# Performance work log

Measured on AMD Instinct MI355X. Metric: run time of the kernel, lower is better.

The kernel has to match this reference:

```python
import jax, jax.numpy as jnp
import numpy as np

B = 65536      # batch
S = 256        # state_dim
A = 8          # n_agents
NA = 16        # n_actions
K = 10         # num_kernel
H = 64         # adv_hypernet_embed
AD = A * NA    # action_dim
D = S + AD     # state_dim + action_dim


def setup_inputs() -> dict:
    key = jax.random.key(0)
    ks = jax.random.split(key, 20)
    sc = 0.05
    inp = {
        'states': jax.random.normal(ks[0], (B, S), jnp.float32),
        'actions_onehot': jax.random.uniform(ks[1], (B, A, NA), jnp.float32),
        # key extractors: S -> H -> H -> 1, stacked over K kernels
        'kW1': jax.random.normal(ks[2], (K, H, S), jnp.float32) * sc,
        'kb1': jnp.zeros((K, H), jnp.float32),
        'kW2': jax.random.normal(ks[3], (K, H, H), jnp.float32) * sc,
        'kb2': jnp.zeros((K, H), jnp.float32),
        'kW3': jax.random.normal(ks[4], (K, 1, H), jnp.float32) * sc,
        'kb3': jnp.zeros((K, 1), jnp.float32),
        # agents extractors: S -> H -> H -> A
        'aW1': jax.random.normal(ks[5], (K, H, S), jnp.float32) * sc,
        'ab1': jnp.zeros((K, H), jnp.float32),
        'aW2': jax.random.normal(ks[6], (K, H, H), jnp.float32) * sc,
        'ab2': jnp.zeros((K, H), jnp.float32),
        'aW3': jax.random.normal(ks[7], (K, A, H), jnp.float32) * sc,
        'ab3': jnp.zeros((K, A), jnp.float32),
        # action extractors: S+AD -> H -> H -> A
        'cW1': jax.random.normal(ks[8], (K, H, D), jnp.float32) * sc,
        'cb1': jnp.zeros((K, H), jnp.float32),
        'cW2': jax.random.normal(ks[9], (K, H, H), jnp.float32) * sc,
        'cb2': jnp.zeros((K, H), jnp.float32),
        'cW3': jax.random.normal(ks[10], (K, A, H), jnp.float32) * sc,
        'cb3': jnp.zeros((K, A), jnp.float32),
    }
    return inp


def _mlp3(x, W1, b1, W2, b2, W3, b3):
    # x: [B, in] ; W1: [K, H, in] -> batched over K kernels in one GEMM
    h = jax.nn.relu(jnp.einsum('bd,khd->bkh', x, W1) + b1)        # [B,K,H]
    h = jax.nn.relu(jnp.einsum('bkh,kgh->bkg', h, W2) + b2)       # [B,K,H]
    return jnp.einsum('bkh,koh->bko', h, W3) + b3                 # [B,K,out]


def reference(states, actions_onehot,
              kW1, kb1, kW2, kb2, kW3, kb3,
              aW1, ab1, aW2, ab2, aW3, ab3,
              cW1, cb1, cW2, cb2, cW3, cb3):
    actions_flat = actions_onehot.reshape(states.shape[0], -1)    # [B, A*NA]
    data = jnp.concatenate([states, actions_flat], axis=1)        # [B, S+AD]

    x_key = jnp.abs(_mlp3(states, kW1, kb1, kW2, kb2, kW3, kb3)) + 1e-10   # [B,K,1]
    x_agents = jax.nn.sigmoid(_mlp3(states, aW1, ab1, aW2, ab2, aW3, ab3)) # [B,K,A]
    x_action = jax.nn.sigmoid(_mlp3(data, cW1, cb1, cW2, cb2, cW3, cb3))   # [B,K,A]

    # broadcast key over agents, multiply gates, sum over the K kernels
    head_attend = jnp.sum(x_key * x_agents * x_action, axis=1)    # [B,A]
    return head_attend
```

## Files before the change

### kernel.cpp

```cpp
#include <hip/hip_runtime.h>
#include <hip/hip_bf16.h>

#define Bsz 65536
#define Sdim 256
#define Aag 8
#define NAct 16
#define Kk 10
#define Hh 64
#define ADdim 128
#define Ddim 384

#define OFF_KW1 0
#define OFF_AW1 16384
#define OFF_CW1 32768
#define OFF_KW2 57344
#define OFF_AW2 61440
#define OFF_CW2 65536
#define OFF_KW3 69632
#define OFF_AW3 70656
#define OFF_CW3 71680
#define SLAB 72704

typedef float f32x4 __attribute__((ext_vector_type(4)));
typedef __bf16 bf16x8 __attribute__((ext_vector_type(8)));

#define MFMA(a, b, cacc) __builtin_amdgcn_mfma_f32_16x16x32_bf16((a), (b), (cacc), 0, 0, 0)

__device__ __forceinline__ __bf16 f2bf(float f) {
    unsigned int u = __float_as_uint(f);
    unsigned int r = (u + 0x7fffu + ((u >> 16) & 1u)) >> 16;
    union { unsigned short s; __bf16 b; } cv;
    cv.s = (unsigned short)r;
    return cv.b;
}

__global__ void prep_weights(const float* __restrict__ kW1, const float* __restrict__ aW1,
                             const float* __restrict__ cW1, const float* __restrict__ kW2,
                             const float* __restrict__ aW2, const float* __restrict__ cW2,
                             const float* __restrict__ kW3, const float* __restrict__ aW3,
                             const float* __restrict__ cW3, __bf16* __restrict__ out) {
    int gid = blockIdx.x * 256 + threadIdx.x;
    if (gid >= SLAB * Kk) return;
    int k = gid / SLAB;
    int off = gid - k * SLAB;
    float v;
    if (off < OFF_AW1)        v = kW1[k * 16384 + off];
    else if (off < OFF_CW1)   v = aW1[k * 16384 + off - OFF_AW1];
    else if (off < OFF_KW2)   v = cW1[k * 24576 + off - OFF_CW1];
    else if (off < OFF_AW2)   v = kW2[k * 4096 + off - OFF_KW2];
    else if (off < OFF_CW2)   v = aW2[k * 4096 + off - OFF_AW2];
    else if (off < OFF_KW3)   v = cW2[k * 4096 + off - OFF_CW2];
    else if (off < OFF_AW3) { int r = off - OFF_KW3; v = (r < 64)  ? kW3[k * 64 + r]  : 0.0f; }
    else if (off < OFF_CW3) { int r = off - OFF_AW3; v = (r < 512) ? aW3[k * 512 + r] : 0.0f; }
    else                    { int r = off - OFF_CW3; v = (r < 512) ? cW3[k * 512 + r] : 0.0f; }
    out[gid] = f2bf(v);
}

template <int KN>
__device__ __forceinline__ void stage_net(const __bf16* __restrict__ w1src,
                                          const __bf16* __restrict__ w2src,
                                          const __bf16* __restrict__ w3src,
                                          __bf16* W1s, __bf16* W2s, __bf16* W3s, int tid) {
    __syncthreads();
    constexpr int STR = KN + 8;
    constexpr int CPR = KN / 8;
    constexpr int N1 = 64 * CPR;
#pragma unroll 4
    for (int ci = tid; ci < N1; ci += 256) {
        int row = ci / CPR;
        int cc = ci - row * CPR;
        *(float4*)(W1s + row * STR + cc * 8) = *(const float4*)(w1src + row * KN + cc * 8);
    }
    {
        int ci = tid;
#pragma unroll
        for (int it = 0; it < 2; ++it, ci += 256) {
            int row = ci >> 3, cc = ci & 7;
            *(float4*)(W2s + row * 72 + cc * 8) = *(const float4*)(w2src + row * 64 + cc * 8);
        }
    }
    if (tid < 128) {
        int row = tid >> 3, cc = tid & 7;
        *(float4*)(W3s + row * 72 + cc * 8) = *(const float4*)(w3src + row * 64 + cc * 8);
    }
    __syncthreads();
}

template <int KB, int MODE>
__device__ __forceinline__ void run_net(const bf16x8 (&xf)[2][12],
                                        const __bf16* W1s, const __bf16* W2s, const __bf16* W3s,
                                        __bf16* hs, int wave, int q, int c, int k, int lane,
                                        const float* __restrict__ b1p, const float* __restrict__ b2p,
                                        const float* __restrict__ b3p,
                                        float (&keyv)[2][4], float (&ag)[2][4], float (&outacc)[2][4]) {
    constexpr int STR = KB * 32 + 8;
    f32x4 acc[2][4];
#pragma unroll
    for (int nt = 0; nt < 4; ++nt) {
        float b = b1p[k * 64 + nt * 16 + c];
        f32x4 bv = {b, b, b, b};
        acc[0][nt] = bv;
        acc[1][nt] = bv;
    }
#pragma unroll
    for (int kb = 0; kb < KB; ++kb) {
        bf16x8 a0 = xf[0][kb];
        bf16x8 a1 = xf[1][kb];
#pragma unroll
        for (int nt = 0; nt < 4; ++nt) {
            bf16x8 bfr = *(const bf16x8*)(W1s + (nt * 16 + c) * STR + kb * 32 + q * 8);
            acc[0][nt] = MFMA(a0, bfr, acc[0][nt]);
            acc[1][nt] = MFMA(a1, bfr, acc[1][nt]);
        }
    }
#pragma unroll
    for (int t = 0; t < 2; ++t) {
        int rb = wave * 32 + t * 16 + q * 4;
#pragma unroll
        for (int nt = 0; nt < 4; ++nt)
#pragma unroll
            for (int i = 0; i < 4; ++i)
                hs[(rb + i) * 72 + nt * 16 + c] = f2bf(fmaxf(acc[t][nt][i], 0.0f));
    }
    f32x4 acc2[2][4];
#pragma unroll
    for (int nt = 0; nt < 4; ++nt) {
        float b = b2p[k * 64 + nt * 16 + c];
        f32x4 bv = {b, b, b, b};
        acc2[0][nt] = bv;
        acc2[1][nt] = bv;
    }
#pragma unroll
    for (int kb = 0; kb < 2; ++kb) {
        bf16x8 a0 = *(const bf16x8*)(hs + (wave * 32 + c) * 72 + kb * 32 + q * 8);
        bf16x8 a1 = *(const bf16x8*)(hs + (wave * 32 + 16 + c) * 72 + kb * 32 + q * 8);
#pragma unroll
        for (int nt = 0; nt < 4; ++nt) {
            bf16x8 bfr = *(const bf16x8*)(W2s + (nt * 16 + c) * 72 + kb * 32 + q * 8);
            acc2[0][nt] = MFMA(a0, bfr, acc2[0][nt]);
            acc2[1][nt] = MFMA(a1, bfr, acc2[1][nt]);
        }
    }
#pragma unroll
    for (int t = 0; t < 2; ++t) {
        int rb = wave * 32 + t * 16 + q * 4;
#pragma unroll
        for (int nt = 0; nt < 4; ++nt)
#pragma unroll
            for (int i = 0; i < 4; ++i)
                hs[(rb + i) * 72 + nt * 16 + c] = f2bf(fmaxf(acc2[t][nt][i], 0.0f));
    }
    f32x4 acc3[2];
    {
        float b3 = (MODE == 0) ? b3p[k] : ((c < 8) ? b3p[k * 8 + c] : 0.0f);
        f32x4 bv = {b3, b3, b3, b3};
        acc3[0] = bv;
        acc3[1] = bv;
    }
#pragma unroll
    for (int kb = 0; kb < 2; ++kb) {
        bf16x8 bfr = *(const bf16x8*)(W3s + c * 72 + kb * 32 + q * 8);
        bf16x8 a0 = *(const bf16x8*)(hs + (wave * 32 + c) * 72 + kb * 32 + q * 8);
        bf16x8 a1 = *(const bf16x8*)(hs + (wave * 32 + 16 + c) * 72 + kb * 32 + q * 8);
        acc3[0] = MFMA(a0, bfr, acc3[0]);
        acc3[1] = MFMA(a1, bfr, acc3[1]);
    }
#pragma unroll
    for (int t = 0; t < 2; ++t)
#pragma unroll
        for (int i = 0; i < 4; ++i) {
            if (MODE == 0) {
                float v = fabsf(acc3[t][i]) + 1e-10f;
                keyv[t][i] = __shfl(v, lane & 48, 64);
            } else if (MODE == 1) {
                ag[t][i] = 1.0f / (1.0f + __expf(-acc3[t][i]));
            } else {
                float s = 1.0f / (1.0f + __expf(-acc3[t][i]));
                outacc[t][i] += keyv[t][i] * ag[t][i] * s;
            }
        }
}

__global__ __launch_bounds__(256, 2) void qplex_main(
    const float* __restrict__ states, const float* __restrict__ actions,
    const __bf16* __restrict__ wbf,
    const float* __restrict__ kb1, const float* __restrict__ kb2, const float* __restrict__ kb3,
    const float* __restrict__ ab1, const float* __restrict__ ab2, const float* __restrict__ ab3,
    const float* __restrict__ cb1, const float* __restrict__ cb2, const float* __restrict__ cb3,
    float* __restrict__ out) {
    __shared__ __bf16 W1s[64 * 392];
    __shared__ __bf16 W2s[64 * 72];
    __shared__ __bf16 W3s[16 * 72];
    __shared__ __bf16 hs[128 * 72];

    const int tid = threadIdx.x;
    const int lane = tid & 63;
    const int wave = tid >> 6;
    const int q = lane >> 4;
    const int c = lane & 15;

    bf16x8 xf[2][12];
#pragma unroll
    for (int t = 0; t < 2; ++t) {
        int r = blockIdx.x * 128 + wave * 32 + t * 16 + c;
        const float* srow = states + (size_t)r * Sdim;
        const float* arow = actions + (size_t)r * ADdim;
#pragma unroll
        for (int kb = 0; kb < 12; ++kb) {
            const float* p = (kb < 8) ? (srow + kb * 32 + q * 8) : (arow + (kb - 8) * 32 + q * 8);
            float4 lo = *(const float4*)p;
            float4 hi = *(const float4*)(p + 4);
            bf16x8 v;
            v[0] = f2bf(lo.x); v[1] = f2bf(lo.y); v[2] = f2bf(lo.z); v[3] = f2bf(lo.w);
            v[4] = f2bf(hi.x); v[5] = f2bf(hi.y); v[6] = f2bf(hi.z); v[7] = f2bf(hi.w);
            xf[t][kb] = v;
        }
    }

    float keyv[2][4], ag[2][4], outacc[2][4];
#pragma unroll
    for (int t = 0; t < 2; ++t)
#pragma unroll
        for (int i = 0; i < 4; ++i) outacc[t][i] = 0.0f;

    for (int k = 0; k < Kk; ++k) {
        const __bf16* slab = wbf + (size_t)k * SLAB;
        stage_net<256>(slab + OFF_KW1, slab + OFF_KW2, slab + OFF_KW3, W1s, W2s, W3s, tid);
        run_net<8, 0>(xf, W1s, W2s, W3s, hs, wave, q, c, k, lane, kb1, kb2, kb3, keyv, ag, outacc);
        stage_net<256>(slab + OFF_AW1, slab + OFF_AW2, slab + OFF_AW3, W1s, W2s, W3s, tid);
        run_net<8, 1>(xf, W1s, W2s, W3s, hs, wave, q, c, k, lane, ab1, ab2, ab3, keyv, ag, outacc);
        stage_net<384>(slab + OFF_CW1, slab + OFF_CW2, slab + OFF_CW3, W1s, W2s, W3s, tid);
        run_net<12, 2>(xf, W1s, W2s, W3s, hs, wave, q, c, k, lane, cb1, cb2, cb3, keyv, ag, outacc);
    }

    if (c < 8) {
#pragma unroll
        for (int t = 0; t < 2; ++t)
#pragma unroll
            for (int i = 0; i < 4; ++i) {
                int r = blockIdx.x * 128 + wave * 32 + t * 16 + q * 4 + i;
                out[(size_t)r * Aag + c] = outacc[t][i];
            }
    }
}

extern "C" void kernel_launch(void* const* d_in, const int* in_sizes, int n_in,
                              void* d_out, int out_size, void* d_ws, size_t ws_size,
                              hipStream_t stream) {
    const float* states = (const float*)d_in[0];
    const float* actions = (const float*)d_in[1];
    const float* kW1 = (const float*)d_in[2];
    const float* kb1 = (const float*)d_in[3];
    const float* kW2 = (const float*)d_in[4];
    const float* kb2 = (const float*)d_in[5];
    const float* kW3 = (const float*)d_in[6];
    const float* kb3 = (const float*)d_in[7];
    const float* aW1 = (const float*)d_in[8];
    const float* ab1 = (const float*)d_in[9];
    const float* aW2 = (const float*)d_in[10];
    const float* ab2 = (const float*)d_in[11];
    const float* aW3 = (const float*)d_in[12];
    const float* ab3 = (const float*)d_in[13];
    const float* cW1 = (const float*)d_in[14];
    const float* cb1 = (const float*)d_in[15];
    const float* cW2 = (const float*)d_in[16];
    const float* cb2 = (const float*)d_in[17];
    const float* cW3 = (const float*)d_in[18];
    const float* cb3 = (const float*)d_in[19];
    float* out = (float*)d_out;
    __bf16* wbf = (__bf16*)d_ws;

    prep_weights<<<(SLAB * Kk + 255) / 256, 256, 0, stream>>>(kW1, aW1, cW1, kW2, aW2, cW2,
                                                              kW3, aW3, cW3, wbf);
    qplex_main<<<Bsz / 128, 256, 0, stream>>>(states, actions, wbf, kb1, kb2, kb3,
                                              ab1, ab2, ab3, cb1, cb2, cb3, out);
}
```

Measured before the change: 304.0 us.

## Double-buffer weights via async global-to-LDS loads and keep activations in registers

Rewrites the main kernel to use 512-thread blocks and two LDS weight buffers. The next network's weights are prefetched with global_load_lds while the current one computes. The GEMMs are transposed so weights form the A operand and the batch forms the B operand, which lets hidden activations stay packed in registers across layers instead of round-tripping through shared memory. prep_weights now writes a row-permuted, XOR-swizzled layout to avoid bank conflicts. This removes the synchronous staging stalls and the LDS traffic for activations, at the cost of more LDS (about 116 KB) and register pressure, and only 256 blocks.

```diff
diff --git a/kernel.cpp b/kernel.cpp
--- a/kernel.cpp
+++ b/kernel.cpp
@@ -4,22 +4,11 @@
 #define Bsz 65536
 #define Sdim 256
 #define Aag 8
-#define NAct 16
 #define Kk 10
-#define Hh 64
 #define ADdim 128
-#define Ddim 384
-
-#define OFF_KW1 0
-#define OFF_AW1 16384
-#define OFF_CW1 32768
-#define OFF_KW2 57344
-#define OFF_AW2 61440
-#define OFF_CW2 65536
-#define OFF_KW3 69632
-#define OFF_AW3 70656
-#define OFF_CW3 71680
-#define SLAB 72704
+
+#define SLAB_K_ELEMS 72704
+#define NET_ELEMS 21504
 
 typedef float f32x4 __attribute__((ext_vector_type(4)));
 typedef __bf16 bf16x8 __attribute__((ext_vector_type(8)));
@@ -34,164 +23,186 @@
     return cv.b;
 }
 
+__device__ __forceinline__ unsigned int pack_bf2(float a, float b) {
+    union { unsigned short s[2]; unsigned int u; } cv;
+    union { unsigned short s; __bf16 b; } x;
+    x.b = f2bf(a); cv.s[0] = x.s;
+    x.b = f2bf(b); cv.s[1] = x.s;
+    return cv.u;
+}
+
+__device__ __forceinline__ int gperm(int n) {
+    return ((n >> 5) << 5) + (((n >> 2) & 3) << 3) + (((n >> 4) & 1) << 2) + (n & 3);
+}
+
 __global__ void prep_weights(const float* __restrict__ kW1, const float* __restrict__ aW1,
                              const float* __restrict__ cW1, const float* __restrict__ kW2,
                              const float* __restrict__ aW2, const float* __restrict__ cW2,
                              const float* __restrict__ kW3, const float* __restrict__ aW3,
                              const float* __restrict__ cW3, __bf16* __restrict__ out) {
     int gid = blockIdx.x * 256 + threadIdx.x;
-    if (gid >= SLAB * Kk) return;
-    int k = gid / SLAB;
-    int off = gid - k * SLAB;
-    float v;
-    if (off < OFF_AW1)        v = kW1[k * 16384 + off];
-    else if (off < OFF_CW1)   v = aW1[k * 16384 + off - OFF_AW1];
-    else if (off < OFF_KW2)   v = cW1[k * 24576 + off - OFF_CW1];
-    else if (off < OFF_AW2)   v = kW2[k * 4096 + off - OFF_KW2];
-    else if (off < OFF_CW2)   v = aW2[k * 4096 + off - OFF_AW2];
-    else if (off < OFF_KW3)   v = cW2[k * 4096 + off - OFF_CW2];
-    else if (off < OFF_AW3) { int r = off - OFF_KW3; v = (r < 64)  ? kW3[k * 64 + r]  : 0.0f; }
-    else if (off < OFF_CW3) { int r = off - OFF_AW3; v = (r < 512) ? aW3[k * 512 + r] : 0.0f; }
-    else                    { int r = off - OFF_CW3; v = (r < 512) ? cW3[k * 512 + r] : 0.0f; }
-    out[gid] = f2bf(v);
-}
-
-template <int KN>
-__device__ __forceinline__ void stage_net(const __bf16* __restrict__ w1src,
-                                          const __bf16* __restrict__ w2src,
-                                          const __bf16* __restrict__ w3src,
-                                          __bf16* W1s, __bf16* W2s, __bf16* W3s, int tid) {
-    __syncthreads();
-    constexpr int STR = KN + 8;
-    constexpr int CPR = KN / 8;
-    constexpr int N1 = 64 * CPR;
-#pragma unroll 4
-    for (int ci = tid; ci < N1; ci += 256) {
-        int row = ci / CPR;
-        int cc = ci - row * CPR;
-        *(float4*)(W1s + row * STR + cc * 8) = *(const float4*)(w1src + row * KN + cc * 8);
-    }
-    {
-        int ci = tid;
-#pragma unroll
-        for (int it = 0; it < 2; ++it, ci += 256) {
-            int row = ci >> 3, cc = ci & 7;
-            *(float4*)(W2s + row * 72 + cc * 8) = *(const float4*)(w2src + row * 64 + cc * 8);
-        }
-    }
-    if (tid < 128) {
-        int row = tid >> 3, cc = tid & 7;
-        *(float4*)(W3s + row * 72 + cc * 8) = *(const float4*)(w3src + row * 64 + cc * 8);
-    }
-    __syncthreads();
+    if (gid >= 90880) return;
+    int k = gid / 9088;
+    int r = gid - k * 9088;
+    int t, cn;
+    if (r < 2688)      { t = 0; cn = r; }
+    else if (r < 5376) { t = 1; cn = r - 2688; }
+    else               { t = 2; cn = r - 5376; }
+    const int KN = (t == 2) ? 384 : 256;
+    const int CPR = KN / 8;
+    const float* W1 = (t == 0) ? kW1 : (t == 1) ? aW1 : cW1;
+    const float* W2 = (t == 0) ? kW2 : (t == 1) ? aW2 : cW2;
+    const float* W3 = (t == 0) ? kW3 : (t == 1) ? aW3 : cW3;
+    const int rows3 = (t == 0) ? 1 : 8;
+    int dstchunk;
+    const float* src = nullptr;
+    if (cn < 64 * CPR) {
+        int n = cn / CPR, k8 = cn - n * CPR;
+        src = W1 + ((size_t)(k * 64 + gperm(n))) * KN + k8 * 8;
+        dstchunk = n * CPR + (k8 ^ (n & 7));
+    } else if (cn < 64 * CPR + 512) {
+        int c2 = cn - 64 * CPR;
+        int n = c2 >> 3, k8 = c2 & 7;
+        src = W2 + ((size_t)(k * 64 + gperm(n))) * 64 + k8 * 8;
+        dstchunk = 64 * CPR + n * 8 + (k8 ^ (n & 7));
+    } else {
+        int c3 = cn - 64 * CPR - 512;
+        int n = c3 >> 3, k8 = c3 & 7;
+        if (n < rows3) src = W3 + ((size_t)(k * rows3 + n)) * 64 + k8 * 8;
+        dstchunk = 64 * CPR + 512 + n * 8 + (k8 ^ (n & 7));
+    }
+    bf16x8 v;
+#pragma unroll
+    for (int e = 0; e < 8; ++e) v[e] = src ? f2bf(src[e]) : (__bf16)0.0f;
+    *(bf16x8*)(out + (size_t)k * SLAB_K_ELEMS + t * NET_ELEMS + dstchunk * 8) = v;
+}
+
+__device__ __forceinline__ void stage(const __bf16* __restrict__ src, __bf16* dst,
+                                      int nchunks, int wave, int lane) {
+    const char* g = (const char*)src + lane * 16;
+    for (int ci = wave; ci < nchunks; ci += 8) {
+        __builtin_amdgcn_global_load_lds(
+            (const __attribute__((address_space(1))) void*)(g + ci * 1024),
+            (__attribute__((address_space(3))) void*)((char*)dst + ci * 1024), 16, 0, 0);
+    }
+}
+
+__device__ __forceinline__ bf16x8 frag_from_hp(const unsigned int (&hp)[4][2], int kb) {
+    int4 u = {(int)hp[kb * 2][0], (int)hp[kb * 2][1], (int)hp[kb * 2 + 1][0], (int)hp[kb * 2 + 1][1]};
+    return __builtin_bit_cast(bf16x8, u);
 }
 
 template <int KB, int MODE>
-__device__ __forceinline__ void run_net(const bf16x8 (&xf)[2][12],
-                                        const __bf16* W1s, const __bf16* W2s, const __bf16* W3s,
-                                        __bf16* hs, int wave, int q, int c, int k, int lane,
-                                        const float* __restrict__ b1p, const float* __restrict__ b2p,
-                                        const float* __restrict__ b3p,
-                                        float (&keyv)[2][4], float (&ag)[2][4], float (&outacc)[2][4]) {
-    constexpr int STR = KB * 32 + 8;
-    f32x4 acc[2][4];
-#pragma unroll
-    for (int nt = 0; nt < 4; ++nt) {
-        float b = b1p[k * 64 + nt * 16 + c];
-        f32x4 bv = {b, b, b, b};
-        acc[0][nt] = bv;
-        acc[1][nt] = bv;
+__device__ __forceinline__ void compute_net(
+    const __bf16* __restrict__ W, const bf16x8 (&xf)[2][12], int q, int c, int k,
+    const float* __restrict__ b1p, const float* __restrict__ b2p, const float* __restrict__ b3p,
+    float (&keyv)[2], float (&ag)[2][4], float (&outacc)[2][4]) {
+    constexpr int CPR = KB * 4;
+    constexpr int W2O = 64 * CPR * 8;
+    constexpr int W3O = W2O + 4096;
+
+    f32x4 acc[4][2];
+#pragma unroll
+    for (int mt = 0; mt < 4; ++mt) {
+        int base = ((mt >> 1) << 5) + (q << 3) + ((mt & 1) << 2);
+        float4 bv = *(const float4*)(b1p + k * 64 + base);
+        f32x4 b = {bv.x, bv.y, bv.z, bv.w};
+        acc[mt][0] = b; acc[mt][1] = b;
     }
 #pragma unroll
     for (int kb = 0; kb < KB; ++kb) {
-        bf16x8 a0 = xf[0][kb];
-        bf16x8 a1 = xf[1][kb];
-#pragma unroll
-        for (int nt = 0; nt < 4; ++nt) {
-            bf16x8 bfr = *(const bf16x8*)(W1s + (nt * 16 + c) * STR + kb * 32 + q * 8);
-            acc[0][nt] = MFMA(a0, bfr, acc[0][nt]);
-            acc[1][nt] = MFMA(a1, bfr, acc[1][nt]);
-        }
-    }
-#pragma unroll
-    for (int t = 0; t < 2; ++t) {
-        int rb = wave * 32 + t * 16 + q * 4;
-#pragma unroll
-        for (int nt = 0; nt < 4; ++nt)
+#pragma unroll
+        for (int mt = 0; mt < 4; ++mt) {
+            int n = mt * 16 + c;
+            bf16x8 a = *(const bf16x8*)(W + ((n * CPR + ((kb * 4 + q) ^ (n & 7))) << 3));
+            acc[mt][0] = MFMA(a, xf[0][kb], acc[mt][0]);
+            acc[mt][1] = MFMA(a, xf[1][kb], acc[mt][1]);
+        }
+    }
+    unsigned int hp[2][4][2];
+#pragma unroll
+    for (int s = 0; s < 2; ++s)
+#pragma unroll
+        for (int mt = 0; mt < 4; ++mt) {
+            hp[s][mt][0] = pack_bf2(fmaxf(acc[mt][s][0], 0.f), fmaxf(acc[mt][s][1], 0.f));
+            hp[s][mt][1] = pack_bf2(fmaxf(acc[mt][s][2], 0.f), fmaxf(acc[mt][s][3], 0.f));
+        }
+
+    f32x4 acc2[4][2];
+#pragma unroll
+    for (int mt = 0; mt < 4; ++mt) {
+        int base = ((mt >> 1) << 5) + (q << 3) + ((mt & 1) << 2);
+        float4 bv = *(const float4*)(b2p + k * 64 + base);
+        f32x4 b = {bv.x, bv.y, bv.z, bv.w};
+        acc2[mt][0] = b; acc2[mt][1] = b;
+    }
+#pragma unroll
+    for (int kb = 0; kb < 2; ++kb) {
+        bf16x8 a2[4];
+#pragma unroll
+        for (int mt = 0; mt < 4; ++mt) {
+            int n = mt * 16 + c;
+            a2[mt] = *(const bf16x8*)(W + W2O + ((n * 8 + ((kb * 4 + q) ^ (n & 7))) << 3));
+        }
+#pragma unroll
+        for (int s = 0; s < 2; ++s) {
+            bf16x8 bh = frag_from_hp(hp[s], kb);
+#pragma unroll
+            for (int mt = 0; mt < 4; ++mt) acc2[mt][s] = MFMA(a2[mt], bh, acc2[mt][s]);
+        }
+    }
+#pragma unroll
+    for (int s = 0; s < 2; ++s)
+#pragma unroll
+        for (int mt = 0; mt < 4; ++mt) {
+            hp[s][mt][0] = pack_bf2(fmaxf(acc2[mt][s][0], 0.f), fmaxf(acc2[mt][s][1], 0.f));
+            hp[s][mt][1] = pack_bf2(fmaxf(acc2[mt][s][2], 0.f), fmaxf(acc2[mt][s][3], 0.f));
+        }
+
+    f32x4 acc3[2];
+    if (MODE == 0) {
+        float b3 = b3p[k];
+        f32x4 z = {0.f, 0.f, 0.f, 0.f};
+        if (q == 0) z[0] = b3;
+        acc3[0] = z; acc3[1] = z;
+    } else {
+        f32x4 z = {0.f, 0.f, 0.f, 0.f};
+        if (q < 2) {
+            float4 bv = *(const float4*)(b3p + k * 8 + q * 4);
+            z = {bv.x, bv.y, bv.z, bv.w};
+        }
+        acc3[0] = z; acc3[1] = z;
+    }
+#pragma unroll
+    for (int kb = 0; kb < 2; ++kb) {
+        bf16x8 a3 = *(const bf16x8*)(W + W3O + ((c * 8 + ((kb * 4 + q) ^ (c & 7))) << 3));
+#pragma unroll
+        for (int s = 0; s < 2; ++s) acc3[s] = MFMA(a3, frag_from_hp(hp[s], kb), acc3[s]);
+    }
+#pragma unroll
+    for (int s = 0; s < 2; ++s) {
+        if (MODE == 0) {
+            float v = __shfl(acc3[s][0], c, 64);
+            keyv[s] = fabsf(v) + 1e-10f;
+        } else if (MODE == 1) {
+#pragma unroll
+            for (int i = 0; i < 4; ++i) ag[s][i] = 1.f / (1.f + __expf(-acc3[s][i]));
+        } else {
 #pragma unroll
             for (int i = 0; i < 4; ++i)
-                hs[(rb + i) * 72 + nt * 16 + c] = f2bf(fmaxf(acc[t][nt][i], 0.0f));
-    }
-    f32x4 acc2[2][4];
-#pragma unroll
-    for (int nt = 0; nt < 4; ++nt) {
-        float b = b2p[k * 64 + nt * 16 + c];
-        f32x4 bv = {b, b, b, b};
-        acc2[0][nt] = bv;
-        acc2[1][nt] = bv;
-    }
-#pragma unroll
-    for (int kb = 0; kb < 2; ++kb) {
-        bf16x8 a0 = *(const bf16x8*)(hs + (wave * 32 + c) * 72 + kb * 32 + q * 8);
-        bf16x8 a1 = *(const bf16x8*)(hs + (wave * 32 + 16 + c) * 72 + kb * 32 + q * 8);
-#pragma unroll
-        for (int nt = 0; nt < 4; ++nt) {
-            bf16x8 bfr = *(const bf16x8*)(W2s + (nt * 16 + c) * 72 + kb * 32 + q * 8);
-            acc2[0][nt] = MFMA(a0, bfr, acc2[0][nt]);
-            acc2[1][nt] = MFMA(a1, bfr, acc2[1][nt]);
-        }
-    }
-#pragma unroll
-    for (int t = 0; t < 2; ++t) {
-        int rb = wave * 32 + t * 16 + q * 4;
-#pragma unroll
-        for (int nt = 0; nt < 4; ++nt)
-#pragma unroll
-            for (int i = 0; i < 4; ++i)
-                hs[(rb + i) * 72 + nt * 16 + c] = f2bf(fmaxf(acc2[t][nt][i], 0.0f));
-    }
-    f32x4 acc3[2];
-    {
-        float b3 = (MODE == 0) ? b3p[k] : ((c < 8) ? b3p[k * 8 + c] : 0.0f);
-        f32x4 bv = {b3, b3, b3, b3};
-        acc3[0] = bv;
-        acc3[1] = bv;
-    }
-#pragma unroll
-    for (int kb = 0; kb < 2; ++kb) {
-        bf16x8 bfr = *(const bf16x8*)(W3s + c * 72 + kb * 32 + q * 8);
-        bf16x8 a0 = *(const bf16x8*)(hs + (wave * 32 + c) * 72 + kb * 32 + q * 8);
-        bf16x8 a1 = *(const bf16x8*)(hs + (wave * 32 + 16 + c) * 72 + kb * 32 + q * 8);
-        acc3[0] = MFMA(a0, bfr, acc3[0]);
-        acc3[1] = MFMA(a1, bfr, acc3[1]);
-    }
-#pragma unroll
-    for (int t = 0; t < 2; ++t)
-#pragma unroll
-        for (int i = 0; i < 4; ++i) {
-            if (MODE == 0) {
-                float v = fabsf(acc3[t][i]) + 1e-10f;
-                keyv[t][i] = __shfl(v, lane & 48, 64);
-            } else if (MODE == 1) {
-                ag[t][i] = 1.0f / (1.0f + __expf(-acc3[t][i]));
-            } else {
-                float s = 1.0f / (1.0f + __expf(-acc3[t][i]));
-                outacc[t][i] += keyv[t][i] * ag[t][i] * s;
-            }
-        }
-}
-
-__global__ __launch_bounds__(256, 2) void qplex_main(
+                outacc[s][i] += keyv[s] * ag[s][i] * (1.f / (1.f + __expf(-acc3[s][i])));
+        }
+    }
+}
+
+__global__ __launch_bounds__(512, 2) void qplex_main(
     const float* __restrict__ states, const float* __restrict__ actions,
     const __bf16* __restrict__ wbf,
-    const float* __restrict__ kb1, const float* __restrict__ kb2, const float* __restrict__ kb3,
-    const float* __restrict__ ab1, const float* __restrict__ ab2, const float* __restrict__ ab3,
-    const float* __restrict__ cb1, const float* __restrict__ cb2, const float* __restrict__ cb3,
+    const float* __restrict__ b1k, const float* __restrict__ b2k, const float* __restrict__ b3k,
+    const float* __restrict__ b1a, const float* __restrict__ b2a, const float* __restrict__ b3a,
+    const float* __restrict__ b1c, const float* __restrict__ b2c, const float* __restrict__ b3c,
     float* __restrict__ out) {
-    __shared__ __bf16 W1s[64 * 392];
-    __shared__ __bf16 W2s[64 * 72];
-    __shared__ __bf16 W3s[16 * 72];
-    __shared__ __bf16 hs[128 * 72];
+    __shared__ __bf16 WB[2][29696];
 
     const int tid = threadIdx.x;
     const int lane = tid & 63;
@@ -199,10 +210,12 @@
     const int q = lane >> 4;
     const int c = lane & 15;
 
+    stage(wbf, WB[0], 42, wave, lane);
+
     bf16x8 xf[2][12];
 #pragma unroll
-    for (int t = 0; t < 2; ++t) {
-        int r = blockIdx.x * 128 + wave * 32 + t * 16 + c;
+    for (int s = 0; s < 2; ++s) {
+        int r = blockIdx.x * 256 + wave * 32 + s * 16 + c;
         const float* srow = states + (size_t)r * Sdim;
         const float* arow = actions + (size_t)r * ADdim;
 #pragma unroll
@@ -213,34 +226,42 @@
             bf16x8 v;
             v[0] = f2bf(lo.x); v[1] = f2bf(lo.y); v[2] = f2bf(lo.z); v[3] = f2bf(lo.w);
             v[4] = f2bf(hi.x); v[5] = f2bf(hi.y); v[6] = f2bf(hi.z); v[7] = f2bf(hi.w);
-            xf[t][kb] = v;
-        }
-    }
-
-    float keyv[2][4], ag[2][4], outacc[2][4];
-#pragma unroll
-    for (int t = 0; t < 2; ++t)
-#pragma unroll
-        for (int i = 0; i < 4; ++i) outacc[t][i] = 0.0f;
+            xf[s][kb] = v;
+        }
+    }
+
+    float keyv[2];
+    float ag[2][4];
+    float outacc[2][4];
+#pragma unroll
+    for (int s = 0; s < 2; ++s) {
+        keyv[s] = 0.f;
+#pragma unroll
+        for (int i = 0; i < 4; ++i) { ag[s][i] = 0.f; outacc[s][i] = 0.f; }
+    }
+
+    __syncthreads();
 
     for (int k = 0; k < Kk; ++k) {
-        const __bf16* slab = wbf + (size_t)k * SLAB;
-        stage_net<256>(slab + OFF_KW1, slab + OFF_KW2, slab + OFF_KW3, W1s, W2s, W3s, tid);
-        run_net<8, 0>(xf, W1s, W2s, W3s, hs, wave, q, c, k, lane, kb1, kb2, kb3, keyv, ag, outacc);
-        stage_net<256>(slab + OFF_AW1, slab + OFF_AW2, slab + OFF_AW3, W1s, W2s, W3s, tid);
-        run_net<8, 1>(xf, W1s, W2s, W3s, hs, wave, q, c, k, lane, ab1, ab2, ab3, keyv, ag, outacc);
-        stage_net<384>(slab + OFF_CW1, slab + OFF_CW2, slab + OFF_CW3, W1s, W2s, W3s, tid);
-        run_net<12, 2>(xf, W1s, W2s, W3s, hs, wave, q, c, k, lane, cb1, cb2, cb3, keyv, ag, outacc);
-    }
-
-    if (c < 8) {
-#pragma unroll
-        for (int t = 0; t < 2; ++t)
-#pragma unroll
-            for (int i = 0; i < 4; ++i) {
-                int r = blockIdx.x * 128 + wave * 32 + t * 16 + q * 4 + i;
-                out[(size_t)r * Aag + c] = outacc[t][i];
-            }
+        const __bf16* kslab = wbf + (size_t)k * SLAB_K_ELEMS;
+        stage(kslab + NET_ELEMS, WB[(k + 1) & 1], 42, wave, lane);
+        compute_net<8, 0>(&WB[k & 1][0], xf, q, c, k, b1k, b2k, b3k, keyv, ag, outacc);
+        __syncthreads();
+        stage(kslab + 2 * NET_ELEMS, WB[k & 1], 58, wave, lane);
+        compute_net<8, 1>(&WB[(k + 1) & 1][0], xf, q, c, k, b1a, b2a, b3a, keyv, ag, outacc);
+        __syncthreads();
+        if (k < Kk - 1) stage(kslab + SLAB_K_ELEMS, WB[(k + 1) & 1], 42, wave, lane);
+        compute_net<12, 2>(&WB[k & 1][0], xf, q, c, k, b1c, b2c, b3c, keyv, ag, outacc);
+        __syncthreads();
+    }
+
+    if (q < 2) {
+#pragma unroll
+        for (int s = 0; s < 2; ++s) {
+            int r = blockIdx.x * 256 + wave * 32 + s * 16 + c;
+            float4 v = {outacc[s][0], outacc[s][1], outacc[s][2], outacc[s][3]};
+            *(float4*)(out + (size_t)r * Aag + q * 4) = v;
+        }
     }
 }
 
@@ -270,8 +291,7 @@
     float* out = (float*)d_out;
     __bf16* wbf = (__bf16*)d_ws;
 
-    prep_weights<<<(SLAB * Kk + 255) / 256, 256, 0, stream>>>(kW1, aW1, cW1, kW2, aW2, cW2,
-                                                              kW3, aW3, cW3, wbf);
-    qplex_main<<<Bsz / 128, 256, 0, stream>>>(states, actions, wbf, kb1, kb2, kb3,
-                                              ab1, ab2, ab3, cb1, cb2, cb3, out);
-}
+    prep_weights<<<355, 256, 0, stream>>>(kW1, aW1, cW1, kW2, aW2, cW2, kW3, aW3, cW3, wbf);
+    qplex_main<<<256, 512, 0, stream>>>(states, actions, wbf, kb1, kb2, kb3,
+                                        ab1, ab2, ab3, cb1, cb2, cb3, out);
+}
```

Measured after the change: 311.2 us. 2.4% more time.
